# Performance work log

Hardware: AMD Instinct MI355X
Metric: run time of the kernel (lower is better)

Reference implementation:

```python
import jax, jax.numpy as jnp
import numpy as np

WIN = 7            # window side -> K2 = 49
DIM = 512          # channel dim C
HEADS = 16
E = DIM // HEADS   # embed_dim / head_dim = 32
SCALE = E ** -0.5


def _rel_pos_index(wh, ww):
    coords = np.stack(np.meshgrid(np.arange(wh), np.arange(ww), indexing='ij'))  # [2, wh, ww]
    cf = coords.reshape(2, -1)                      # [2, K2]
    rel = cf[:, :, None] - cf[:, None, :]           # [2, K2, K2]
    rel = rel.transpose(1, 2, 0).astype(np.int64)   # [K2, K2, 2]
    rel[..., 0] += wh - 1
    rel[..., 1] += ww - 1
    rel[..., 0] *= 2 * ww - 1
    return rel.sum(-1)                              # [K2, K2]

RPI = jnp.asarray(_rel_pos_index(WIN, WIN))         # constant int index map


def setup_inputs() -> dict:
    key = jax.random.key(0)
    ks = jax.random.split(key, 9)
    s = 0.02
    return {
        'x':         jax.random.normal(ks[0], (2048, WIN * WIN, DIM), jnp.float32),
        'qk_w':      jax.random.normal(ks[1], (2 * DIM, DIM), jnp.float32) * s,
        'qk_b':      jnp.zeros((2 * DIM,), jnp.float32),
        'rev_v_w':   jax.random.normal(ks[2], (DIM, DIM), jnp.float32) * s,
        'rev_v_b':   jnp.zeros((DIM,), jnp.float32),
        'wg_w':      jax.random.normal(ks[3], (E * E, DIM), jnp.float32) * s,
        'proj_w':    jax.random.normal(ks[4], (DIM, DIM), jnp.float32) * s,
        'proj_b':    jnp.zeros((DIM,), jnp.float32),
        'rpb_table': jax.random.normal(ks[5], ((2 * WIN - 1) ** 2, HEADS), jnp.float32) * s,
    }


def reference(x, qk_w, qk_b, rev_v_w, rev_v_b, wg_w, proj_w, proj_b, rpb_table):
    BW, K2, C = x.shape
    # joint q/k projection: [BW, K2, 2, H, E]
    qk = (x @ qk_w.T + qk_b).reshape(BW, K2, 2, HEADS, E)
    q = qk[:, :, 0].transpose(0, 2, 1, 3) * SCALE   # [BW, H, K2, E]
    k = qk[:, :, 1].transpose(0, 2, 1, 3)           # [BW, H, K2, E]
    attn = jnp.einsum('bhqe,bhke->bhqk', q, k)      # [BW, H, K2, K2]
    # relative position bias gather: [K2, K2, H] -> [H, K2, K2]
    bias = rpb_table[RPI].transpose(2, 0, 1)
    attn = jax.nn.softmax(attn + bias[None], axis=-1)
    # reverse attention: values projected, softmax transposed (transpose_softmax=True)
    v = (x @ rev_v_w.T + rev_v_b).reshape(BW, K2, HEADS, E).transpose(0, 2, 1, 3)  # [BW, H, K2, E]
    expert_mixture = jnp.einsum('bhkq,bhke->bhqe', attn, v)   # attn^T @ v, [BW, H, K2, E]
    # hypernetwork: per-token E x E mixing matrices from the raw input
    proj_weight = (x @ wg_w.T).reshape(BW, K2, E, E)          # [BW, K2, E, E]
    em_t = expert_mixture.transpose(0, 2, 1, 3)               # [BW, K2, H, E]
    out = jnp.einsum('bkhe,bkef->bkhf', em_t, proj_weight).reshape(BW, K2, C)
    # output projection (reverse_proj); dropouts are identity (p=0)
    return out @ proj_w.T + proj_b
```

## Files before the change

kernel.cpp:

```cpp
#include <hip/hip_runtime.h>
#include <hip/hip_bf16.h>
#include <stdint.h>

typedef __attribute__((ext_vector_type(8))) short short8;
typedef __attribute__((ext_vector_type(4))) float f32x4;
typedef unsigned short u16;

#define SCALE_F 0.17677669529663687f

__device__ __forceinline__ u16 f2bf(float f){
  union { float f; unsigned u; } x; x.f = f;
  unsigned r = x.u + 0x7fffu + ((x.u >> 16) & 1u);
  return (u16)(r >> 16);
}
__device__ __forceinline__ float bf2f(u16 u){
  union { float f; unsigned u; } x; x.u = ((unsigned)u) << 16; return x.f;
}
__device__ __forceinline__ unsigned swz(unsigned base, int row, unsigned rowb, unsigned colb){
  return base + (unsigned)row * rowb + (colb ^ (((unsigned)row & 7u) << 4));
}
__device__ __forceinline__ void gll16(const void* g, void* l){
  __builtin_amdgcn_global_load_lds(
    (const __attribute__((address_space(1))) unsigned int*)(unsigned long long)(size_t)g,
    (__attribute__((address_space(3))) unsigned int*)(unsigned int)(size_t)l,
    16, 0, 0);
}

__global__ void convk(const float* __restrict__ x,
                      const float* __restrict__ qk_w, const float* __restrict__ rev_v_w,
                      const float* __restrict__ wg_w, const float* __restrict__ proj_w,
                      u16* __restrict__ ws){
  long long i8 = ((long long)blockIdx.x * 256 + threadIdx.x) * 8;
  const float* s;
  if      (i8 <  524288) s = qk_w   + i8;
  else if (i8 <  786432) s = rev_v_w + (i8 - 524288);
  else if (i8 < 1310720) s = wg_w   + (i8 - 786432);
  else if (i8 < 1572864) s = proj_w + (i8 - 1310720);
  else                   s = x      + (i8 - 1572864);
  f32x4 lo = *(const f32x4*)s, hi = *(const f32x4*)(s + 4);
  short8 v;
  v[0]=f2bf(lo[0]); v[1]=f2bf(lo[1]); v[2]=f2bf(lo[2]); v[3]=f2bf(lo[3]);
  v[4]=f2bf(hi[0]); v[5]=f2bf(hi[1]); v[6]=f2bf(hi[2]); v[7]=f2bf(hi[3]);
  *(short8*)(ws + i8) = v;
}

template<int NT, int F32OUT>
__global__ __launch_bounds__(256, 2)
void gemm128(const u16* __restrict__ A, int lda,
             const u16* __restrict__ B,
             const float* __restrict__ b0, const float* __restrict__ b1,
             void* __restrict__ Cg, int ldc){
  __shared__ __align__(16) unsigned char sm[32768];
  const int tid = threadIdx.x, wave = tid >> 6, lane = tid & 63;
  const int l15 = lane & 15, lg = lane >> 4;
  const int nwg = gridDim.x, bidr = blockIdx.x;
  const int q8 = nwg >> 3, r8 = nwg & 7, xc = bidr & 7, oo = bidr >> 3;
  const int wg = (xc < r8 ? xc * (q8 + 1) : r8 * (q8 + 1) + (xc - r8) * q8) + oo;
  const int bm = wg / NT, bn = wg % NT;
  const int wm = wave >> 1, wn = wave & 1;
  const f32x4 zf = {0.f, 0.f, 0.f, 0.f};
  f32x4 acc[4][4];
#pragma unroll
  for (int mt=0; mt<4; mt++)
#pragma unroll
    for (int nt=0; nt<4; nt++) acc[mt][nt] = zf;

  const u16* Ab = A + (size_t)bm * 128 * lda;
  const u16* Bb = B + (size_t)bn * 128 * 512;

  for (int ks = 0; ks < 8; ks++){
#pragma unroll
    for (int it = 0; it < 4; it++){
      int c = (wave*4 + it)*64 + lane;
      int r = c >> 3, cc = c & 7;
      int sc = cc ^ (r & 7);
      gll16(Ab + (size_t)r*lda + ks*64 + sc*8, sm + (unsigned)(wave*4 + it)*1024u);
      gll16(Bb + (size_t)r*512 + ks*64 + sc*8, sm + 16384u + (unsigned)(wave*4 + it)*1024u);
    }
    __syncthreads();
#pragma unroll
    for (int kk = 0; kk < 2; kk++){
      short8 aq[4], bq[4];
#pragma unroll
      for (int mt=0; mt<4; mt++){
        int r = wm*64 + mt*16 + l15;
        aq[mt] = *(const short8*)(sm + (unsigned)r*128u + (((unsigned)(kk*64 + lg*16)) ^ (((unsigned)r & 7u) << 4)));
      }
#pragma unroll
      for (int nt=0; nt<4; nt++){
        int r = wn*64 + nt*16 + l15;
        bq[nt] = *(const short8*)(sm + 16384u + (unsigned)r*128u + (((unsigned)(kk*64 + lg*16)) ^ (((unsigned)r & 7u) << 4)));
      }
#pragma unroll
      for (int mt=0; mt<4; mt++)
#pragma unroll
        for (int nt=0; nt<4; nt++)
          acc[mt][nt] = __builtin_amdgcn_mfma_f32_16x16x32_bf16(aq[mt], bq[nt], acc[mt][nt], 0, 0, 0);
    }
    __syncthreads();
  }

  float bia[4];
#pragma unroll
  for (int nt=0; nt<4; nt++){
    int n = bn*128 + wn*64 + nt*16 + l15;
    if (F32OUT) bia[nt] = b0[n];
    else        bia[nt] = (n < 1024) ? b0[n] : (n < 1536 ? b1[n - 1024] : 0.f);
  }

  if (!F32OUT){
#pragma unroll
    for (int mt=0; mt<4; mt++)
#pragma unroll
      for (int nt=0; nt<4; nt++)
#pragma unroll
        for (int i=0; i<4; i++){
          int row = wm*64 + mt*16 + lg*4 + i;
          unsigned colb = (unsigned)((wn*64 + nt*16 + l15) * 2);
          *(u16*)(sm + (unsigned)row*256u + (colb ^ (((unsigned)row & 7u) << 4))) = f2bf(acc[mt][nt][i] + bia[nt]);
        }
    __syncthreads();
    u16* Co = (u16*)Cg;
#pragma unroll
    for (int it=0; it<8; it++){
      int c = it*256 + tid;
      int r = c >> 4, cc = c & 15;
      short8 v = *(const short8*)(sm + (unsigned)r*256u + (((unsigned)(cc*16)) ^ (((unsigned)r & 7u) << 4)));
      *(short8*)(Co + (size_t)(bm*128 + r)*ldc + bn*128 + cc*8) = v;
    }
  } else {
    float* Co = (float*)Cg;
#pragma unroll
    for (int half=0; half<2; half++){
      if (wm == half){
#pragma unroll
        for (int mt=0; mt<4; mt++)
#pragma unroll
          for (int nt=0; nt<4; nt++)
#pragma unroll
            for (int i=0; i<4; i++){
              int row = mt*16 + lg*4 + i;
              unsigned colb = (unsigned)((wn*64 + nt*16 + l15) * 4);
              *(float*)(sm + (unsigned)row*512u + (colb ^ (((unsigned)row & 7u) << 4))) = acc[mt][nt][i] + bia[nt];
            }
      }
      __syncthreads();
#pragma unroll
      for (int it=0; it<8; it++){
        int c = it*256 + tid;
        int r = c >> 5, cc = c & 31;
        f32x4 v = *(const f32x4*)(sm + (unsigned)r*512u + (((unsigned)(cc*16)) ^ (((unsigned)r & 7u) << 4)));
        *(f32x4*)(Co + (size_t)(bm*128 + half*64 + r)*ldc + bn*128 + cc*4) = v;
      }
      __syncthreads();
    }
  }
}

__global__ __launch_bounds__(512, 4)
void attn_half(const u16* __restrict__ qkv, const float* __restrict__ rpb,
               u16* __restrict__ em){
  __shared__ __align__(16) unsigned char lds[77968];
  const unsigned L_V = 0u, L_PT = 25088u, L_RPB = 75264u;
  const int tid = threadIdx.x, wave = tid >> 6, lane = tid & 63;
  const int l15 = lane & 15, lg = lane >> 4;
  const int bid = blockIdx.x, win = bid >> 1, hf = bid & 1;
  const u16* base = qkv + (size_t)win * 49 * 2560;
  u16* emb = em + (size_t)win * 49 * 512 + hf * 256;
  unsigned char* ptb = lds + L_PT + (unsigned)wave * 6272u;
  const int h = hf*8 + wave;
  const f32x4 zf = {0.f, 0.f, 0.f, 0.f};

  for (int i = tid; i < 169*8; i += 512){
    int idx = i >> 3, hh = i & 7;
    *(u16*)(lds + L_RPB + i*2) = f2bf(rpb[idx*16 + hf*8 + hh]);
  }
  for (int c = tid; c < 49*32; c += 512){
    int r = c >> 5, c8 = c & 31;
    short8 v = *(const short8*)(base + (size_t)r*2560 + 1024 + hf*256 + c8*8);
    *(short8*)(lds + swz(L_V, r, 512u, (unsigned)(c8*16))) = v;
  }
  __syncthreads();

  short8 aq[4], bq[4];
#pragma unroll
  for (int mt=0; mt<4; mt++){
    int r = mt*16 + l15; if (r > 48) r = 48;
    aq[mt] = *(const short8*)(base + (size_t)r*2560 + h*32 + lg*8);
  }
#pragma unroll
  for (int nt=0; nt<4; nt++){
    int kt = nt*16 + l15; if (kt > 48) kt = 48;
    bq[nt] = *(const short8*)(base + (size_t)kt*2560 + 512 + h*32 + lg*8);
  }
  f32x4 s[4][4];
#pragma unroll
  for (int mt=0; mt<4; mt++)
#pragma unroll
    for (int nt=0; nt<4; nt++) s[mt][nt] = zf;
#pragma unroll
  for (int mt=0; mt<4; mt++)
#pragma unroll
    for (int nt=0; nt<4; nt++)
      s[mt][nt] = __builtin_amdgcn_mfma_f32_16x16x32_bf16(aq[mt], bq[nt], s[mt][nt], 0, 0, 0);
#pragma unroll
  for (int mt=0; mt<4; mt++)
#pragma unroll
    for (int nt=0; nt<4; nt++)
#pragma unroll
      for (int i=0; i<4; i++){
        int q  = mt*16 + lg*4 + i;
        int kt = nt*16 + l15;
        float v = s[mt][nt][i] * SCALE_F;
        if (kt < 49){
          int qc = (q > 48) ? 48 : q;
          int qi = qc / 7, qj = qc - qi*7;
          int ki = kt / 7, kj = kt - ki*7;
          int idx = (qi - ki + 6)*13 + (qj - kj + 6);
          v += bf2f(*(const u16*)(lds + L_RPB + (idx*8 + wave)*2));
        } else v = -1e30f;
        s[mt][nt][i] = v;
      }
#pragma unroll
  for (int mt=0; mt<4; mt++)
#pragma unroll
    for (int i=0; i<4; i++){
      float m = fmaxf(fmaxf(s[mt][0][i], s[mt][1][i]), fmaxf(s[mt][2][i], s[mt][3][i]));
      m = fmaxf(m, __shfl_xor(m, 1)); m = fmaxf(m, __shfl_xor(m, 2));
      m = fmaxf(m, __shfl_xor(m, 4)); m = fmaxf(m, __shfl_xor(m, 8));
      float sum = 0.f;
#pragma unroll
      for (int nt=0; nt<4; nt++){ float e = __expf(s[mt][nt][i] - m); s[mt][nt][i] = e; sum += e; }
      sum += __shfl_xor(sum, 1); sum += __shfl_xor(sum, 2);
      sum += __shfl_xor(sum, 4); sum += __shfl_xor(sum, 8);
      float inv = 1.0f / sum;
#pragma unroll
      for (int nt=0; nt<4; nt++) s[mt][nt][i] *= inv;
    }
#pragma unroll
  for (int mt=0; mt<4; mt++)
#pragma unroll
    for (int nt=0; nt<4; nt++)
#pragma unroll
      for (int i=0; i<4; i++){
        int q  = mt*16 + lg*4 + i;
        int kt = nt*16 + l15;
        if (kt < 49){
          u16 val = (q < 49) ? f2bf(s[mt][nt][i]) : (u16)0;
          *(u16*)(ptb + (unsigned)kt*128u + (((unsigned)(q*2)) ^ (((unsigned)kt & 7u) << 4))) = val;
        }
      }
  f32x4 emv[4][2];
#pragma unroll
  for (int mt=0; mt<4; mt++)
#pragma unroll
    for (int nt=0; nt<2; nt++) emv[mt][nt] = zf;
#pragma unroll
  for (int kk=0; kk<2; kk++){
    short8 pa[4];
#pragma unroll
    for (int mt=0; mt<4; mt++){
      int r = mt*16 + l15; if (r > 48) r = 48;
      pa[mt] = *(const short8*)(ptb + (unsigned)r*128u + (((unsigned)(kk*64 + lg*16)) ^ (((unsigned)r & 7u) << 4)));
    }
    short8 vb[2];
#pragma unroll
    for (int nt=0; nt<2; nt++){
      int chl = wave*32 + nt*16 + l15;
#pragma unroll
      for (int j=0; j<8; j++){
        int kt = kk*32 + lg*8 + j; if (kt > 48) kt = 48;
        vb[nt][j] = *(const short*)(lds + swz(L_V, kt, 512u, (unsigned)(chl*2)));
      }
    }
#pragma unroll
    for (int mt=0; mt<4; mt++)
#pragma unroll
      for (int nt=0; nt<2; nt++)
        emv[mt][nt] = __builtin_amdgcn_mfma_f32_16x16x32_bf16(pa[mt], vb[nt], emv[mt][nt], 0, 0, 0);
  }
#pragma unroll
  for (int mt=0; mt<4; mt++)
#pragma unroll
    for (int nt=0; nt<2; nt++)
#pragma unroll
      for (int i=0; i<4; i++){
        int q = mt*16 + lg*4 + i;
        if (q < 49)
          emb[(size_t)q*512 + wave*32 + nt*16 + l15] = f2bf(emv[mt][nt][i]);
      }
}

__global__ __launch_bounds__(512, 4)
void hyper2(const u16* __restrict__ qkvpw, const u16* __restrict__ em,
            u16* __restrict__ o1){
  __shared__ __align__(16) unsigned char lds[16384];
  const int tid = threadIdx.x, wave = tid >> 6, lane = tid & 63;
  const int l15 = lane & 15, lg = lane >> 4;
  unsigned char* pwb = lds + (unsigned)wave * 2048u;
  const size_t t = (size_t)blockIdx.x * 8 + wave;
  const u16* pwt = qkvpw + t*2560 + 1536;
  const u16* emt = em + t*512;
  const f32x4 zf = {0.f, 0.f, 0.f, 0.f};

#pragma unroll
  for (int rd = 0; rd < 2; rd++){
    int i8 = (rd*64 + lane)*8;
    short8 v = *(const short8*)(pwt + i8);
    int e = i8 >> 5, f0 = i8 & 31;
#pragma unroll
    for (int jj = 0; jj < 8; jj++){
      int f = f0 + jj;
      *(u16*)(pwb + (unsigned)f*64u + (((unsigned)(e*2)) ^ (((unsigned)f & 3u) << 4))) = (u16)v[jj];
    }
  }
  short8 ea = *(const short8*)(emt + l15*32 + lg*8);
  __syncthreads();
  f32x4 o[2];
#pragma unroll
  for (int nt=0; nt<2; nt++){
    int f = nt*16 + l15;
    short8 pb = *(const short8*)(pwb + (unsigned)f*64u + (((unsigned)(lg*16)) ^ (((unsigned)f & 3u) << 4)));
    o[nt] = __builtin_amdgcn_mfma_f32_16x16x32_bf16(ea, pb, zf, 0, 0, 0);
  }
  __syncthreads();
#pragma unroll
  for (int nt=0; nt<2; nt++)
#pragma unroll
    for (int i=0; i<4; i++){
      int ch = (lg*4 + i)*32 + nt*16 + l15;
      *(u16*)(pwb + (unsigned)ch*2u) = f2bf(o[nt][i]);
    }
  __syncthreads();
  short8 v = *(const short8*)(pwb + (unsigned)lane*16u);
  *(short8*)(o1 + t*512 + lane*8) = v;
}

#define LDS_X   0u
#define LDS_V   50176u
#define LDS_QK  100352u
#define LDS_RPB 150528u
#define LDS_PW  50176u
#define LDS_EM  0u
#define LDS_TOTAL 155936

__device__ __forceinline__ void gemm_strip(const unsigned char* ldsp, unsigned abase,
    const u16* __restrict__ W, int wrow0, int l15, int lg, f32x4 acc[4][4]){
  for (int kk = 0; kk < 16; kk++){
    short8 bq[4];
#pragma unroll
    for (int nt = 0; nt < 4; nt++){
      const u16* p = W + (size_t)(wrow0 + nt*16 + l15) * 512 + kk*32 + lg*8;
      bq[nt] = *(const short8*)p;
    }
    short8 aq[4];
#pragma unroll
    for (int mt = 0; mt < 4; mt++){
      int r = mt*16 + l15; if (r > 48) r = 48;
      aq[mt] = *(const short8*)(ldsp + swz(abase, r, 1024u, (unsigned)(kk*64 + lg*16)));
    }
#pragma unroll
    for (int mt = 0; mt < 4; mt++)
#pragma unroll
      for (int nt = 0; nt < 4; nt++)
        acc[mt][nt] = __builtin_amdgcn_mfma_f32_16x16x32_bf16(aq[mt], bq[nt], acc[mt][nt], 0, 0, 0);
  }
}

__global__ void conv_w4(const float* __restrict__ a, const float* __restrict__ b,
                        const float* __restrict__ c, const float* __restrict__ d,
                        u16* __restrict__ o){
  int i = blockIdx.x * 256 + threadIdx.x;
  if (i < 524288)        o[i] = f2bf(a[i]);
  else if (i < 786432)   o[i] = f2bf(b[i - 524288]);
  else if (i < 1310720)  o[i] = f2bf(c[i - 786432]);
  else                   o[i] = f2bf(d[i - 1310720]);
}

__launch_bounds__(512, 2)
__global__ void wa_main(
    const float* __restrict__ x, const float* __restrict__ qk_b,
    const float* __restrict__ rev_v_b, const float* __restrict__ proj_b,
    const float* __restrict__ rpb,
    const u16* __restrict__ Wqk, const u16* __restrict__ Wv,
    const u16* __restrict__ Wwg, const u16* __restrict__ Wproj,
    float* __restrict__ out){
  __shared__ __align__(16) unsigned char ldsp[LDS_TOTAL];
  const int tid  = threadIdx.x;
  const int wave = tid >> 6, lane = tid & 63, l15 = lane & 15, lg = lane >> 4;
  const int b = blockIdx.x;
  const float* xb = x + (size_t)b * 49 * 512;
  const f32x4 zf = {0.f, 0.f, 0.f, 0.f};
  for (int i = tid; i < 169*16; i += 512)
    *(u16*)(ldsp + LDS_RPB + i*2) = f2bf(rpb[i]);
  for (int ch = tid; ch < 49*64; ch += 512){
    int r = ch >> 6, c8 = ch & 63;
    const f32x4* s = (const f32x4*)(xb + r*512 + c8*8);
    f32x4 lo = s[0], hi = s[1];
    short8 v;
    v[0]=f2bf(lo[0]); v[1]=f2bf(lo[1]); v[2]=f2bf(lo[2]); v[3]=f2bf(lo[3]);
    v[4]=f2bf(hi[0]); v[5]=f2bf(hi[1]); v[6]=f2bf(hi[2]); v[7]=f2bf(hi[3]);
    *(short8*)(ldsp + swz(LDS_X, r, 1024u, (unsigned)(c8*16))) = v;
  }
  __syncthreads();
  {
    f32x4 acc[4][4];
#pragma unroll
    for (int mt=0; mt<4; mt++)
#pragma unroll
      for (int nt=0; nt<4; nt++) acc[mt][nt] = zf;
    gemm_strip(ldsp, LDS_X, Wv, wave*64, l15, lg, acc);
#pragma unroll
    for (int nt=0; nt<4; nt++){
      int ch = wave*64 + nt*16 + l15;
      float bias = rev_v_b[ch];
#pragma unroll
      for (int mt=0; mt<4; mt++)
#pragma unroll
        for (int i=0; i<4; i++){
          int r = mt*16 + lg*4 + i;
          if (r < 49)
            *(u16*)(ldsp + swz(LDS_V, r, 1024u, (unsigned)(ch*2))) = f2bf(acc[mt][nt][i] + bias);
        }
    }
  }
  auto qk_pass = [&](int p){
    f32x4 acc[4][4];
#pragma unroll
    for (int mt=0; mt<4; mt++)
#pragma unroll
      for (int nt=0; nt<4; nt++) acc[mt][nt] = zf;
    int wrow0 = (wave < 4) ? (p*256 + wave*64) : (512 + p*256 + (wave-4)*64);
    gemm_strip(ldsp, LDS_X, Wqk, wrow0, l15, lg, acc);
#pragma unroll
    for (int nt=0; nt<4; nt++){
      int ch  = wrow0 + nt*16 + l15;
      int col = wave*64 + nt*16 + l15;
      float bias = qk_b[ch];
#pragma unroll
      for (int mt=0; mt<4; mt++)
#pragma unroll
        for (int i=0; i<4; i++){
          int r = mt*16 + lg*4 + i;
          if (r < 49)
            *(u16*)(ldsp + swz(LDS_QK, r, 1024u, (unsigned)(col*2))) = f2bf(acc[mt][nt][i] + bias);
        }
    }
  };
  auto attn_pass = [&](int p, f32x4 (&em)[4][2]){
    const int h = p*8 + wave;
    f32x4 s[4][4];
#pragma unroll
    for (int mt=0; mt<4; mt++)
#pragma unroll
      for (int nt=0; nt<4; nt++) s[mt][nt] = zf;
    short8 aq[4], bq[4];
#pragma unroll
    for (int mt=0; mt<4; mt++){
      int r = mt*16 + l15; if (r > 48) r = 48;
      aq[mt] = *(const short8*)(ldsp + swz(LDS_QK, r, 1024u, (unsigned)(wave*64 + lg*16)));
    }
#pragma unroll
    for (int nt=0; nt<4; nt++){
      int kt = nt*16 + l15; if (kt > 48) kt = 48;
      bq[nt] = *(const short8*)(ldsp + swz(LDS_QK, kt, 1024u, (unsigned)(512 + wave*64 + lg*16)));
    }
#pragma unroll
    for (int mt=0; mt<4; mt++)
#pragma unroll
      for (int nt=0; nt<4; nt++)
        s[mt][nt] = __builtin_amdgcn_mfma_f32_16x16x32_bf16(aq[mt], bq[nt], s[mt][nt], 0, 0, 0);
#pragma unroll
    for (int mt=0; mt<4; mt++)
#pragma unroll
      for (int nt=0; nt<4; nt++)
#pragma unroll
        for (int i=0; i<4; i++){
          int q  = mt*16 + lg*4 + i;
          int kt = nt*16 + l15;
          float v = s[mt][nt][i] * SCALE_F;
          if (kt < 49){
            int qc = (q > 48) ? 48 : q;
            int qi = qc / 7, qj = qc - qi*7;
            int ki = kt / 7, kj = kt - ki*7;
            int idx = (qi - ki + 6)*13 + (qj - kj + 6);
            v += bf2f(*(const u16*)(ldsp + LDS_RPB + (idx*16 + h)*2));
          } else v = -1e30f;
          s[mt][nt][i] = v;
        }
#pragma unroll
    for (int mt=0; mt<4; mt++)
#pragma unroll
      for (int i=0; i<4; i++){
        float m = fmaxf(fmaxf(s[mt][0][i], s[mt][1][i]), fmaxf(s[mt][2][i], s[mt][3][i]));
        m = fmaxf(m, __shfl_xor(m, 1)); m = fmaxf(m, __shfl_xor(m, 2));
        m = fmaxf(m, __shfl_xor(m, 4)); m = fmaxf(m, __shfl_xor(m, 8));
        float sum = 0.f;
#pragma unroll
        for (int nt=0; nt<4; nt++){ float e = __expf(s[mt][nt][i] - m); s[mt][nt][i] = e; sum += e; }
        sum += __shfl_xor(sum, 1); sum += __shfl_xor(sum, 2);
        sum += __shfl_xor(sum, 4); sum += __shfl_xor(sum, 8);
        float inv = 1.0f / sum;
#pragma unroll
        for (int nt=0; nt<4; nt++) s[mt][nt][i] *= inv;
      }
    __syncthreads();
    const unsigned ptb = LDS_QK + (unsigned)wave * 6272u;
#pragma unroll
    for (int mt=0; mt<4; mt++)
#pragma unroll
      for (int nt=0; nt<4; nt++)
#pragma unroll
        for (int i=0; i<4; i++){
          int q  = mt*16 + lg*4 + i;
          int kt = nt*16 + l15;
          if (kt < 49){
            u16 val = (q < 49) ? f2bf(s[mt][nt][i]) : (u16)0;
            *(u16*)(ldsp + ptb + (unsigned)kt*128u + (((unsigned)(q*2)) ^ (((unsigned)kt & 7u) << 4))) = val;
          }
        }
#pragma unroll
    for (int kk=0; kk<2; kk++){
      short8 pa[4];
#pragma unroll
      for (int mt=0; mt<4; mt++){
        int r = mt*16 + l15; if (r > 48) r = 48;
        pa[mt] = *(const short8*)(ldsp + ptb + (unsigned)r*128u + (((unsigned)(kk*64 + lg*16)) ^ (((unsigned)r & 7u) << 4)));
      }
      short8 vb[2];
#pragma unroll
      for (int nt=0; nt<2; nt++){
        int ch = h*32 + nt*16 + l15;
#pragma unroll
        for (int j=0; j<8; j++){
          int kt = kk*32 + lg*8 + j; if (kt > 48) kt = 48;
          vb[nt][j] = *(const short*)(ldsp + swz(LDS_V, kt, 1024u, (unsigned)(ch*2)));
        }
      }
#pragma unroll
      for (int mt=0; mt<4; mt++)
#pragma unroll
        for (int nt=0; nt<2; nt++)
          em[mt][nt] = __builtin_amdgcn_mfma_f32_16x16x32_bf16(pa[mt], vb[nt], em[mt][nt], 0, 0, 0);
    }
  };
  f32x4 em0[4][2], em1[4][2];
#pragma unroll
  for (int mt=0; mt<4; mt++)
#pragma unroll
    for (int nt=0; nt<2; nt++){ em0[mt][nt] = zf; em1[mt][nt] = zf; }
  qk_pass(0);
  __syncthreads();
  attn_pass(0, em0);
  __syncthreads();
  qk_pass(1);
  __syncthreads();
  attn_pass(1, em1);
  __syncthreads();
  for (int nh = 0; nh < 2; nh++){
    f32x4 acc[4][4];
#pragma unroll
    for (int mt=0; mt<4; mt++)
#pragma unroll
      for (int nt=0; nt<4; nt++) acc[mt][nt] = zf;
    int n0 = nh*512 + wave*64;
    gemm_strip(ldsp, LDS_X, Wwg, n0, l15, lg, acc);
#pragma unroll
    for (int nt=0; nt<4; nt++){
      int n  = n0 + nt*16 + l15;
      int pc = (n & 31)*32 + (n >> 5);
      unsigned cb = ((unsigned)(pc*2)) ^ (((unsigned)n & 7u) << 4);
#pragma unroll
      for (int mt=0; mt<4; mt++)
#pragma unroll
        for (int i=0; i<4; i++){
          int r = mt*16 + lg*4 + i;
          if (r < 49)
            *(u16*)(ldsp + LDS_PW + (unsigned)r*2048u + cb) = f2bf(acc[mt][nt][i]);
        }
    }
  }
  __syncthreads();
  auto em_store = [&](f32x4 (&em)[4][2], int h){
#pragma unroll
    for (int mt=0; mt<4; mt++)
#pragma unroll
      for (int nt=0; nt<2; nt++)
#pragma unroll
        for (int i=0; i<4; i++){
          int q = mt*16 + lg*4 + i;
          if (q < 49){
            int ch = h*32 + nt*16 + l15;
            *(u16*)(ldsp + swz(LDS_EM, q, 1024u, (unsigned)(ch*2))) = f2bf(em[mt][nt][i]);
          }
        }
  };
  em_store(em0, wave);
  em_store(em1, 8 + wave);
  __syncthreads();
  for (int t = wave; t < 49; t += 8){
    short8 ea = *(const short8*)(ldsp + swz(LDS_EM, t, 1024u, (unsigned)(l15*64 + lg*16)));
    f32x4 o[2];
#pragma unroll
    for (int nt=0; nt<2; nt++){
      int f = nt*16 + l15;
      short8 pb = *(const short8*)(ldsp + LDS_PW + (unsigned)t*2048u +
                    (((unsigned)((f*32 + lg*8)*2)) ^ (((unsigned)f & 7u) << 4)));
      o[nt] = __builtin_amdgcn_mfma_f32_16x16x32_bf16(ea, pb, zf, 0, 0, 0);
    }
#pragma unroll
    for (int nt=0; nt<2; nt++)
#pragma unroll
      for (int i=0; i<4; i++){
        int h2 = lg*4 + i;
        int ch = h2*32 + nt*16 + l15;
        *(u16*)(ldsp + swz(LDS_EM, t, 1024u, (unsigned)(ch*2))) = f2bf(o[nt][i]);
      }
  }
  __syncthreads();
  {
    f32x4 acc[4][4];
#pragma unroll
    for (int mt=0; mt<4; mt++)
#pragma unroll
      for (int nt=0; nt<4; nt++) acc[mt][nt] = zf;
    gemm_strip(ldsp, LDS_EM, Wproj, wave*64, l15, lg, acc);
    float* ob = out + (size_t)b * 49 * 512;
#pragma unroll
    for (int nt=0; nt<4; nt++){
      int n = wave*64 + nt*16 + l15;
      float bias = proj_b[n];
#pragma unroll
      for (int mt=0; mt<4; mt++)
#pragma unroll
        for (int i=0; i<4; i++){
          int r = mt*16 + lg*4 + i;
          if (r < 49) ob[r*512 + n] = acc[mt][nt][i] + bias;
        }
    }
  }
}

extern "C" void kernel_launch(void* const* d_in, const int* in_sizes, int n_in,
                              void* d_out, int out_size, void* d_ws, size_t ws_size,
                              hipStream_t stream){
  const float* x       = (const float*)d_in[0];
  const float* qk_w    = (const float*)d_in[1];
  const float* qk_b    = (const float*)d_in[2];
  const float* rev_v_w = (const float*)d_in[3];
  const float* rev_v_b = (const float*)d_in[4];
  const float* wg_w    = (const float*)d_in[5];
  const float* proj_w  = (const float*)d_in[6];
  const float* proj_b  = (const float*)d_in[7];
  const float* rpb     = (const float*)d_in[8];
  u16* ws = (u16*)d_ws;

  const unsigned long long BASE = 105906176ULL;
  int C = 0;
  for (int cand : {512, 1024, 2048, 256, 128}){
    if (BASE + (unsigned long long)cand * 351232ULL <= ws_size){ C = cand; break; }
  }
  if (C == 0){
    conv_w4<<<6144, 256, 0, stream>>>(qk_w, rev_v_w, wg_w, proj_w, ws);
    wa_main<<<2048, 512, 0, stream>>>(x, qk_b, rev_v_b, proj_b, rpb,
        ws, ws + 524288, ws + 786432, ws + 1310720, (float*)d_out);
    return;
  }

  u16* Wcat  = ws;
  u16* Wproj = ws + 1310720;
  u16* xb    = ws + 1572864;
  u16* qkvpw = ws + 52953088ULL;
  u16* o1    = qkvpw + (size_t)C * 49 * 2560;
  u16* em    = o1 + (size_t)C * 49 * 512;

  convk<<<25856, 256, 0, stream>>>(x, qk_w, rev_v_w, wg_w, proj_w, ws);

  const int nch = 2048 / C;
  const int mt128 = C * 49 / 128;
  for (int ch = 0; ch < nch; ch++){
    size_t t0 = (size_t)ch * C * 49;
    gemm128<20, 0><<<mt128 * 20, 256, 0, stream>>>(xb + t0*512, 512, Wcat,
        qk_b, rev_v_b, qkvpw, 2560);
    attn_half<<<2 * C, 512, 0, stream>>>(qkvpw, rpb, em);
    hyper2<<<C * 49 / 8, 512, 0, stream>>>(qkvpw, em, o1);
    gemm128<4, 1><<<mt128 * 4, 256, 0, stream>>>(o1, 512, Wproj,
        proj_b, (const float*)nullptr, (float*)d_out + t0*512, 512);
  }
  (void)Wcat; (void)Wproj;
}
```

Baseline: 666.2 us.

## Fuse hypernetwork mixing into attention kernel, keeping expert mixture in LDS

Removes the separate hyper2 kernel. Each attn_half2 block now writes its expert-mixture tile to shared memory, then loops over the window's 49 tokens. For each token it loads the per-token E×E mixing matrix, runs the small MFMA and writes o1 directly. This cuts the global round-trip of the em buffer and one kernel launch per chunk, and shrinks the workspace requirement. In exchange, both head-halves of a window reload the same per-token mixing matrix, and each wave processes tokens serially inside the block.

```diff
diff --git a/kernel.cpp b/kernel.cpp
--- a/kernel.cpp
+++ b/kernel.cpp
@@ -3,6 +3,7 @@
 #include <stdint.h>
 
 typedef __attribute__((ext_vector_type(8))) short short8;
+typedef __attribute__((ext_vector_type(4))) short s16x4;
 typedef __attribute__((ext_vector_type(4))) float f32x4;
 typedef unsigned short u16;
 
@@ -158,15 +159,14 @@
 }
 
 __global__ __launch_bounds__(512, 4)
-void attn_half(const u16* __restrict__ qkv, const float* __restrict__ rpb,
-               u16* __restrict__ em){
+void attn_half2(const u16* __restrict__ qkv, const float* __restrict__ rpb,
+                u16* __restrict__ o1){
   __shared__ __align__(16) unsigned char lds[77968];
   const unsigned L_V = 0u, L_PT = 25088u, L_RPB = 75264u;
   const int tid = threadIdx.x, wave = tid >> 6, lane = tid & 63;
   const int l15 = lane & 15, lg = lane >> 4;
   const int bid = blockIdx.x, win = bid >> 1, hf = bid & 1;
   const u16* base = qkv + (size_t)win * 49 * 2560;
-  u16* emb = em + (size_t)win * 49 * 512 + hf * 256;
   unsigned char* ptb = lds + L_PT + (unsigned)wave * 6272u;
   const int h = hf*8 + wave;
   const f32x4 zf = {0.f, 0.f, 0.f, 0.f};
@@ -279,6 +279,8 @@
       for (int nt=0; nt<2; nt++)
         emv[mt][nt] = __builtin_amdgcn_mfma_f32_16x16x32_bf16(pa[mt], vb[nt], emv[mt][nt], 0, 0, 0);
   }
+
+  __syncthreads();
 #pragma unroll
   for (int mt=0; mt<4; mt++)
 #pragma unroll
@@ -286,54 +288,46 @@
 #pragma unroll
       for (int i=0; i<4; i++){
         int q = mt*16 + lg*4 + i;
-        if (q < 49)
-          emb[(size_t)q*512 + wave*32 + nt*16 + l15] = f2bf(emv[mt][nt][i]);
-      }
-}
-
-__global__ __launch_bounds__(512, 4)
-void hyper2(const u16* __restrict__ qkvpw, const u16* __restrict__ em,
-            u16* __restrict__ o1){
-  __shared__ __align__(16) unsigned char lds[16384];
-  const int tid = threadIdx.x, wave = tid >> 6, lane = tid & 63;
-  const int l15 = lane & 15, lg = lane >> 4;
-  unsigned char* pwb = lds + (unsigned)wave * 2048u;
-  const size_t t = (size_t)blockIdx.x * 8 + wave;
-  const u16* pwt = qkvpw + t*2560 + 1536;
-  const u16* emt = em + t*512;
-  const f32x4 zf = {0.f, 0.f, 0.f, 0.f};
-
-#pragma unroll
-  for (int rd = 0; rd < 2; rd++){
-    int i8 = (rd*64 + lane)*8;
-    short8 v = *(const short8*)(pwt + i8);
-    int e = i8 >> 5, f0 = i8 & 31;
-#pragma unroll
-    for (int jj = 0; jj < 8; jj++){
-      int f = f0 + jj;
-      *(u16*)(pwb + (unsigned)f*64u + (((unsigned)(e*2)) ^ (((unsigned)f & 3u) << 4))) = (u16)v[jj];
-    }
-  }
-  short8 ea = *(const short8*)(emt + l15*32 + lg*8);
-  __syncthreads();
-  f32x4 o[2];
-#pragma unroll
-  for (int nt=0; nt<2; nt++){
-    int f = nt*16 + l15;
-    short8 pb = *(const short8*)(pwb + (unsigned)f*64u + (((unsigned)(lg*16)) ^ (((unsigned)f & 3u) << 4)));
-    o[nt] = __builtin_amdgcn_mfma_f32_16x16x32_bf16(ea, pb, zf, 0, 0, 0);
-  }
-  __syncthreads();
-#pragma unroll
-  for (int nt=0; nt<2; nt++)
-#pragma unroll
-    for (int i=0; i<4; i++){
-      int ch = (lg*4 + i)*32 + nt*16 + l15;
-      *(u16*)(pwb + (unsigned)ch*2u) = f2bf(o[nt][i]);
-    }
-  __syncthreads();
-  short8 v = *(const short8*)(pwb + (unsigned)lane*16u);
-  *(short8*)(o1 + t*512 + lane*8) = v;
+        if (q < 49){
+          int ch2 = wave*32 + nt*16 + l15;
+          *(u16*)(lds + swz(L_PT, q, 1024u, (unsigned)(ch2*2))) = f2bf(emv[mt][nt][i]);
+        }
+      }
+  __syncthreads();
+
+  unsigned char* pwb = lds + L_V + (unsigned)wave * 2048u;
+  u16* ob = o1 + (size_t)win * 49 * 512 + hf * 256;
+  for (int t = wave; t < 49; t += 8){
+    const u16* pwt = base + (size_t)t*2560 + 1536;
+#pragma unroll
+    for (int rd = 0; rd < 2; rd++){
+      int i8 = (rd*64 + lane)*8;
+      short8 v = *(const short8*)(pwt + i8);
+      int e = i8 >> 5, f0 = i8 & 31;
+#pragma unroll
+      for (int jj = 0; jj < 8; jj++){
+        int f = f0 + jj;
+        *(u16*)(pwb + (unsigned)f*64u + (((unsigned)(e*2)) ^ (((unsigned)f & 3u) << 4))) = (u16)v[jj];
+      }
+    }
+    short8 ea = *(const short8*)(lds + swz(L_PT, t, 1024u, (unsigned)(l15*64 + lg*16)));
+    f32x4 o[2];
+#pragma unroll
+    for (int nt2=0; nt2<2; nt2++){
+      int f = nt2*16 + l15;
+      short8 pb = *(const short8*)(pwb + (unsigned)f*64u + (((unsigned)(lg*16)) ^ (((unsigned)f & 3u) << 4)));
+      o[nt2] = __builtin_amdgcn_mfma_f32_16x16x32_bf16(ea, pb, zf, 0, 0, 0);
+    }
+#pragma unroll
+    for (int nt2=0; nt2<2; nt2++)
+#pragma unroll
+      for (int i=0; i<4; i++){
+        int ch2 = (lg*4 + i)*32 + nt2*16 + l15;
+        *(u16*)(pwb + (unsigned)ch2*2u) = f2bf(o[nt2][i]);
+      }
+    s16x4 ov = *(const s16x4*)(pwb + (unsigned)lane*8u);
+    *(s16x4*)(ob + (size_t)t*512 + lane*4) = ov;
+  }
 }
 
 #define LDS_X   0u
@@ -658,7 +652,7 @@
   const unsigned long long BASE = 105906176ULL;
   int C = 0;
   for (int cand : {512, 1024, 2048, 256, 128}){
-    if (BASE + (unsigned long long)cand * 351232ULL <= ws_size){ C = cand; break; }
+    if (BASE + (unsigned long long)cand * 301056ULL <= ws_size){ C = cand; break; }
   }
   if (C == 0){
     conv_w4<<<6144, 256, 0, stream>>>(qk_w, rev_v_w, wg_w, proj_w, ws);
@@ -672,7 +666,6 @@
   u16* xb    = ws + 1572864;
   u16* qkvpw = ws + 52953088ULL;
   u16* o1    = qkvpw + (size_t)C * 49 * 2560;
-  u16* em    = o1 + (size_t)C * 49 * 512;
 
   convk<<<25856, 256, 0, stream>>>(x, qk_w, rev_v_w, wg_w, proj_w, ws);
 
@@ -682,8 +675,7 @@
     size_t t0 = (size_t)ch * C * 49;
     gemm128<20, 0><<<mt128 * 20, 256, 0, stream>>>(xb + t0*512, 512, Wcat,
         qk_b, rev_v_b, qkvpw, 2560);
-    attn_half<<<2 * C, 512, 0, stream>>>(qkvpw, rpb, em);
-    hyper2<<<C * 49 / 8, 512, 0, stream>>>(qkvpw, em, o1);
+    attn_half2<<<2 * C, 512, 0, stream>>>(qkvpw, rpb, o1);
     gemm128<4, 1><<<mt128 * 4, 256, 0, stream>>>(o1, 512, Wproj,
         proj_b, (const float*)nullptr, (float*)d_out + t0*512, 512);
   }
```

New measurement: 678.5 us. About the same (+1.9%).

## Add 256x256 pipelined GEMM for fused QKV/hypernet projection, drop fallback path

Applied to the files above, without the earlier changes.

Adds a 512-thread GEMM kernel with 256x256 output tiles, double-buffered global-to-LDS direct loads, XOR-swizzled LDS, barrier-phased MFMA with priority bumps, and an LDS-staged coalesced epilogue. It replaces the 128x128 GEMM for the large projection when the row count divides by 256, aiming for more operand reuse and better load/compute overlap. It also removes the old fused single-kernel fallback and the C=2048 chunk option. The larger tile uses 128KB of dynamic LDS and allows one block per CU, which lowers occupancy.

```diff
diff --git a/kernel.cpp b/kernel.cpp
--- a/kernel.cpp
+++ b/kernel.cpp
@@ -44,6 +44,131 @@
   *(short8*)(ws + i8) = v;
 }
 
+template<int NT>
+__global__ __launch_bounds__(512, 1)
+void gemm256p(const u16* __restrict__ A,
+              const u16* __restrict__ B,
+              const float* __restrict__ b0, const float* __restrict__ b1,
+              u16* __restrict__ Cg, int ldc){
+  extern __shared__ __align__(16) unsigned char dyn[];
+  const int tid = threadIdx.x, wave = tid >> 6, lane = tid & 63;
+  const int l15 = lane & 15, lg = lane >> 4;
+  const int nwg = gridDim.x, bidr = blockIdx.x;
+  const int q8 = nwg >> 3, r8 = nwg & 7, xc = bidr & 7, oo = bidr >> 3;
+  const int wg = (xc < r8 ? xc*(q8+1) : r8*(q8+1) + (xc-r8)*q8) + oo;
+  const int bm = wg / NT, bn = wg % NT;
+  const int wm = wave >> 2, wn = wave & 3;
+  const f32x4 zf = {0.f, 0.f, 0.f, 0.f};
+
+  float bia[4];
+#pragma unroll
+  for (int nf=0; nf<4; nf++){
+    int n = bn*256 + wn*64 + nf*16 + l15;
+    bia[nf] = (n < 1024) ? b0[n] : (n < 1536 ? b1[n-1024] : 0.f);
+  }
+  asm volatile("s_waitcnt vmcnt(0)" ::: "memory");
+
+  const u16* Ab = A + (size_t)bm * 256 * 512;
+  const u16* Bb = B + (size_t)bn * 256 * 512;
+
+  const int c0 = tid, c1 = 512 + tid;
+  const int r0s = c0 >> 3, sc0 = (c0 & 7) ^ (r0s & 7);
+  const int r1s = c1 >> 3, sc1 = (c1 & 7) ^ (r1s & 7);
+
+  auto stageA = [&](int t, int h){
+    unsigned slot = ((unsigned)(t & 1)*2u + (unsigned)h) * 16384u;
+    const u16* src = Ab + (size_t)(h*128) * 512 + t*64;
+    gll16(src + (size_t)r0s*512 + sc0*8, dyn + slot + (unsigned)c0*16u);
+    gll16(src + (size_t)r1s*512 + sc1*8, dyn + slot + (unsigned)c1*16u);
+  };
+  auto stageB = [&](int t, int h){
+    unsigned slot = 65536u + ((unsigned)(t & 1)*2u + (unsigned)h) * 16384u;
+    const u16* src = Bb + (size_t)(h*128) * 512 + t*64;
+    gll16(src + (size_t)r0s*512 + sc0*8, dyn + slot + (unsigned)c0*16u);
+    gll16(src + (size_t)r1s*512 + sc1*8, dyn + slot + (unsigned)c1*16u);
+  };
+
+  f32x4 acc[8][4];
+#pragma unroll
+  for (int mf=0; mf<8; mf++)
+#pragma unroll
+    for (int nf=0; nf<4; nf++) acc[mf][nf] = zf;
+
+  stageA(0,0); stageA(0,1); stageB(0,0); stageB(0,1); stageB(1,0); stageB(1,1);
+  asm volatile("s_waitcnt vmcnt(4)" ::: "memory");
+  __builtin_amdgcn_s_barrier();
+  __builtin_amdgcn_sched_barrier(0);
+
+  short8 bq[4][2];
+  for (int t = 0; t < 8; t++){
+    const unsigned aslot = ((unsigned)(t&1)*2u + (unsigned)wm) * 16384u;
+    const unsigned bslot = 65536u + ((unsigned)(t&1)*2u + (unsigned)(wn>>1)) * 16384u;
+    const int brow = (wn & 1)*64;
+#pragma unroll
+    for (int p = 0; p < 4; p++){
+      short8 aq[2][2];
+#pragma unroll
+      for (int j=0; j<2; j++)
+#pragma unroll
+        for (int kk=0; kk<2; kk++){
+          int rl = p*32 + j*16 + l15;
+          aq[j][kk] = *(const short8*)(dyn + aslot + (unsigned)rl*128u +
+                        (((unsigned)(kk*64 + lg*16)) ^ (((unsigned)rl & 7u) << 4)));
+        }
+      if (p == 0){
+#pragma unroll
+        for (int nf=0; nf<4; nf++)
+#pragma unroll
+          for (int kk=0; kk<2; kk++){
+            int rl = brow + nf*16 + l15;
+            bq[nf][kk] = *(const short8*)(dyn + bslot + (unsigned)rl*128u +
+                          (((unsigned)(kk*64 + lg*16)) ^ (((unsigned)rl & 7u) << 4)));
+          }
+      }
+      if (p < 2){ if (t+1 < 8) stageA(t+1, p); }
+      else      { if (t+2 < 8) stageB(t+2, p-2); }
+      if (p == 3){
+        if (t <= 5)      asm volatile("s_waitcnt vmcnt(4)" ::: "memory");
+        else if (t == 6) asm volatile("s_waitcnt vmcnt(0)" ::: "memory");
+      }
+      __builtin_amdgcn_s_barrier();
+      __builtin_amdgcn_sched_barrier(0);
+      __builtin_amdgcn_s_setprio(1);
+#pragma unroll
+      for (int j=0; j<2; j++)
+#pragma unroll
+        for (int nf=0; nf<4; nf++)
+#pragma unroll
+          for (int kk=0; kk<2; kk++)
+            acc[p*2+j][nf] = __builtin_amdgcn_mfma_f32_16x16x32_bf16(
+                                aq[j][kk], bq[nf][kk], acc[p*2+j][nf], 0, 0, 0);
+      __builtin_amdgcn_s_setprio(0);
+      __builtin_amdgcn_s_barrier();
+      __builtin_amdgcn_sched_barrier(0);
+    }
+  }
+
+  __syncthreads();
+#pragma unroll
+  for (int mf=0; mf<8; mf++)
+#pragma unroll
+    for (int nf=0; nf<4; nf++)
+#pragma unroll
+      for (int i=0; i<4; i++){
+        int row = wm*128 + mf*16 + lg*4 + i;
+        unsigned colb = (unsigned)((wn*64 + nf*16 + l15) * 2);
+        *(u16*)(dyn + (unsigned)row*512u + (colb ^ (((unsigned)row & 7u) << 4))) = f2bf(acc[mf][nf][i] + bia[nf]);
+      }
+  __syncthreads();
+#pragma unroll
+  for (int it=0; it<16; it++){
+    int c = it*512 + tid;
+    int r = c >> 5, cc = c & 31;
+    short8 v = *(const short8*)(dyn + (unsigned)r*512u + (((unsigned)(cc*16)) ^ (((unsigned)r & 7u) << 4)));
+    *(short8*)(Cg + (size_t)(bm*256 + r)*ldc + bn*256 + cc*8) = v;
+  }
+}
+
 template<int NT, int F32OUT>
 __global__ __launch_bounds__(256, 2)
 void gemm128(const u16* __restrict__ A, int lda,
@@ -336,311 +461,6 @@
   *(short8*)(o1 + t*512 + lane*8) = v;
 }
 
-#define LDS_X   0u
-#define LDS_V   50176u
-#define LDS_QK  100352u
-#define LDS_RPB 150528u
-#define LDS_PW  50176u
-#define LDS_EM  0u
-#define LDS_TOTAL 155936
-
-__device__ __forceinline__ void gemm_strip(const unsigned char* ldsp, unsigned abase,
-    const u16* __restrict__ W, int wrow0, int l15, int lg, f32x4 acc[4][4]){
-  for (int kk = 0; kk < 16; kk++){
-    short8 bq[4];
-#pragma unroll
-    for (int nt = 0; nt < 4; nt++){
-      const u16* p = W + (size_t)(wrow0 + nt*16 + l15) * 512 + kk*32 + lg*8;
-      bq[nt] = *(const short8*)p;
-    }
-    short8 aq[4];
-#pragma unroll
-    for (int mt = 0; mt < 4; mt++){
-      int r = mt*16 + l15; if (r > 48) r = 48;
-      aq[mt] = *(const short8*)(ldsp + swz(abase, r, 1024u, (unsigned)(kk*64 + lg*16)));
-    }
-#pragma unroll
-    for (int mt = 0; mt < 4; mt++)
-#pragma unroll
-      for (int nt = 0; nt < 4; nt++)
-        acc[mt][nt] = __builtin_amdgcn_mfma_f32_16x16x32_bf16(aq[mt], bq[nt], acc[mt][nt], 0, 0, 0);
-  }
-}
-
-__global__ void conv_w4(const float* __restrict__ a, const float* __restrict__ b,
-                        const float* __restrict__ c, const float* __restrict__ d,
-                        u16* __restrict__ o){
-  int i = blockIdx.x * 256 + threadIdx.x;
-  if (i < 524288)        o[i] = f2bf(a[i]);
-  else if (i < 786432)   o[i] = f2bf(b[i - 524288]);
-  else if (i < 1310720)  o[i] = f2bf(c[i - 786432]);
-  else                   o[i] = f2bf(d[i - 1310720]);
-}
-
-__launch_bounds__(512, 2)
-__global__ void wa_main(
-    const float* __restrict__ x, const float* __restrict__ qk_b,
-    const float* __restrict__ rev_v_b, const float* __restrict__ proj_b,
-    const float* __restrict__ rpb,
-    const u16* __restrict__ Wqk, const u16* __restrict__ Wv,
-    const u16* __restrict__ Wwg, const u16* __restrict__ Wproj,
-    float* __restrict__ out){
-  __shared__ __align__(16) unsigned char ldsp[LDS_TOTAL];
-  const int tid  = threadIdx.x;
-  const int wave = tid >> 6, lane = tid & 63, l15 = lane & 15, lg = lane >> 4;
-  const int b = blockIdx.x;
-  const float* xb = x + (size_t)b * 49 * 512;
-  const f32x4 zf = {0.f, 0.f, 0.f, 0.f};
-  for (int i = tid; i < 169*16; i += 512)
-    *(u16*)(ldsp + LDS_RPB + i*2) = f2bf(rpb[i]);
-  for (int ch = tid; ch < 49*64; ch += 512){
-    int r = ch >> 6, c8 = ch & 63;
-    const f32x4* s = (const f32x4*)(xb + r*512 + c8*8);
-    f32x4 lo = s[0], hi = s[1];
-    short8 v;
-    v[0]=f2bf(lo[0]); v[1]=f2bf(lo[1]); v[2]=f2bf(lo[2]); v[3]=f2bf(lo[3]);
-    v[4]=f2bf(hi[0]); v[5]=f2bf(hi[1]); v[6]=f2bf(hi[2]); v[7]=f2bf(hi[3]);
-    *(short8*)(ldsp + swz(LDS_X, r, 1024u, (unsigned)(c8*16))) = v;
-  }
-  __syncthreads();
-  {
-    f32x4 acc[4][4];
-#pragma unroll
-    for (int mt=0; mt<4; mt++)
-#pragma unroll
-      for (int nt=0; nt<4; nt++) acc[mt][nt] = zf;
-    gemm_strip(ldsp, LDS_X, Wv, wave*64, l15, lg, acc);
-#pragma unroll
-    for (int nt=0; nt<4; nt++){
-      int ch = wave*64 + nt*16 + l15;
-      float bias = rev_v_b[ch];
-#pragma unroll
-      for (int mt=0; mt<4; mt++)
-#pragma unroll
-        for (int i=0; i<4; i++){
-          int r = mt*16 + lg*4 + i;
-          if (r < 49)
-            *(u16*)(ldsp + swz(LDS_V, r, 1024u, (unsigned)(ch*2))) = f2bf(acc[mt][nt][i] + bias);
-        }
-    }
-  }
-  auto qk_pass = [&](int p){
-    f32x4 acc[4][4];
-#pragma unroll
-    for (int mt=0; mt<4; mt++)
-#pragma unroll
-      for (int nt=0; nt<4; nt++) acc[mt][nt] = zf;
-    int wrow0 = (wave < 4) ? (p*256 + wave*64) : (512 + p*256 + (wave-4)*64);
-    gemm_strip(ldsp, LDS_X, Wqk, wrow0, l15, lg, acc);
-#pragma unroll
-    for (int nt=0; nt<4; nt++){
-      int ch  = wrow0 + nt*16 + l15;
-      int col = wave*64 + nt*16 + l15;
-      float bias = qk_b[ch];
-#pragma unroll
-      for (int mt=0; mt<4; mt++)
-#pragma unroll
-        for (int i=0; i<4; i++){
-          int r = mt*16 + lg*4 + i;
-          if (r < 49)
-            *(u16*)(ldsp + swz(LDS_QK, r, 1024u, (unsigned)(col*2))) = f2bf(acc[mt][nt][i] + bias);
-        }
-    }
-  };
-  auto attn_pass = [&](int p, f32x4 (&em)[4][2]){
-    const int h = p*8 + wave;
-    f32x4 s[4][4];
-#pragma unroll
-    for (int mt=0; mt<4; mt++)
-#pragma unroll
-      for (int nt=0; nt<4; nt++) s[mt][nt] = zf;
-    short8 aq[4], bq[4];
-#pragma unroll
-    for (int mt=0; mt<4; mt++){
-      int r = mt*16 + l15; if (r > 48) r = 48;
-      aq[mt] = *(const short8*)(ldsp + swz(LDS_QK, r, 1024u, (unsigned)(wave*64 + lg*16)));
-    }
-#pragma unroll
-    for (int nt=0; nt<4; nt++){
-      int kt = nt*16 + l15; if (kt > 48) kt = 48;
-      bq[nt] = *(const short8*)(ldsp + swz(LDS_QK, kt, 1024u, (unsigned)(512 + wave*64 + lg*16)));
-    }
-#pragma unroll
-    for (int mt=0; mt<4; mt++)
-#pragma unroll
-      for (int nt=0; nt<4; nt++)
-        s[mt][nt] = __builtin_amdgcn_mfma_f32_16x16x32_bf16(aq[mt], bq[nt], s[mt][nt], 0, 0, 0);
-#pragma unroll
-    for (int mt=0; mt<4; mt++)
-#pragma unroll
-      for (int nt=0; nt<4; nt++)
-#pragma unroll
-        for (int i=0; i<4; i++){
-          int q  = mt*16 + lg*4 + i;
-          int kt = nt*16 + l15;
-          float v = s[mt][nt][i] * SCALE_F;
-          if (kt < 49){
-            int qc = (q > 48) ? 48 : q;
-            int qi = qc / 7, qj = qc - qi*7;
-            int ki = kt / 7, kj = kt - ki*7;
-            int idx = (qi - ki + 6)*13 + (qj - kj + 6);
-            v += bf2f(*(const u16*)(ldsp + LDS_RPB + (idx*16 + h)*2));
-          } else v = -1e30f;
-          s[mt][nt][i] = v;
-        }
-#pragma unroll
-    for (int mt=0; mt<4; mt++)
-#pragma unroll
-      for (int i=0; i<4; i++){
-        float m = fmaxf(fmaxf(s[mt][0][i], s[mt][1][i]), fmaxf(s[mt][2][i], s[mt][3][i]));
-        m = fmaxf(m, __shfl_xor(m, 1)); m = fmaxf(m, __shfl_xor(m, 2));
-        m = fmaxf(m, __shfl_xor(m, 4)); m = fmaxf(m, __shfl_xor(m, 8));
-        float sum = 0.f;
-#pragma unroll
-        for (int nt=0; nt<4; nt++){ float e = __expf(s[mt][nt][i] - m); s[mt][nt][i] = e; sum += e; }
-        sum += __shfl_xor(sum, 1); sum += __shfl_xor(sum, 2);
-        sum += __shfl_xor(sum, 4); sum += __shfl_xor(sum, 8);
-        float inv = 1.0f / sum;
-#pragma unroll
-        for (int nt=0; nt<4; nt++) s[mt][nt][i] *= inv;
-      }
-    __syncthreads();
-    const unsigned ptb = LDS_QK + (unsigned)wave * 6272u;
-#pragma unroll
-    for (int mt=0; mt<4; mt++)
-#pragma unroll
-      for (int nt=0; nt<4; nt++)
-#pragma unroll
-        for (int i=0; i<4; i++){
-          int q  = mt*16 + lg*4 + i;
-          int kt = nt*16 + l15;
-          if (kt < 49){
-            u16 val = (q < 49) ? f2bf(s[mt][nt][i]) : (u16)0;
-            *(u16*)(ldsp + ptb + (unsigned)kt*128u + (((unsigned)(q*2)) ^ (((unsigned)kt & 7u) << 4))) = val;
-          }
-        }
-#pragma unroll
-    for (int kk=0; kk<2; kk++){
-      short8 pa[4];
-#pragma unroll
-      for (int mt=0; mt<4; mt++){
-        int r = mt*16 + l15; if (r > 48) r = 48;
-        pa[mt] = *(const short8*)(ldsp + ptb + (unsigned)r*128u + (((unsigned)(kk*64 + lg*16)) ^ (((unsigned)r & 7u) << 4)));
-      }
-      short8 vb[2];
-#pragma unroll
-      for (int nt=0; nt<2; nt++){
-        int ch = h*32 + nt*16 + l15;
-#pragma unroll
-        for (int j=0; j<8; j++){
-          int kt = kk*32 + lg*8 + j; if (kt > 48) kt = 48;
-          vb[nt][j] = *(const short*)(ldsp + swz(LDS_V, kt, 1024u, (unsigned)(ch*2)));
-        }
-      }
-#pragma unroll
-      for (int mt=0; mt<4; mt++)
-#pragma unroll
-        for (int nt=0; nt<2; nt++)
-          em[mt][nt] = __builtin_amdgcn_mfma_f32_16x16x32_bf16(pa[mt], vb[nt], em[mt][nt], 0, 0, 0);
-    }
-  };
-  f32x4 em0[4][2], em1[4][2];
-#pragma unroll
-  for (int mt=0; mt<4; mt++)
-#pragma unroll
-    for (int nt=0; nt<2; nt++){ em0[mt][nt] = zf; em1[mt][nt] = zf; }
-  qk_pass(0);
-  __syncthreads();
-  attn_pass(0, em0);
-  __syncthreads();
-  qk_pass(1);
-  __syncthreads();
-  attn_pass(1, em1);
-  __syncthreads();
-  for (int nh = 0; nh < 2; nh++){
-    f32x4 acc[4][4];
-#pragma unroll
-    for (int mt=0; mt<4; mt++)
-#pragma unroll
-      for (int nt=0; nt<4; nt++) acc[mt][nt] = zf;
-    int n0 = nh*512 + wave*64;
-    gemm_strip(ldsp, LDS_X, Wwg, n0, l15, lg, acc);
-#pragma unroll
-    for (int nt=0; nt<4; nt++){
-      int n  = n0 + nt*16 + l15;
-      int pc = (n & 31)*32 + (n >> 5);
-      unsigned cb = ((unsigned)(pc*2)) ^ (((unsigned)n & 7u) << 4);
-#pragma unroll
-      for (int mt=0; mt<4; mt++)
-#pragma unroll
-        for (int i=0; i<4; i++){
-          int r = mt*16 + lg*4 + i;
-          if (r < 49)
-            *(u16*)(ldsp + LDS_PW + (unsigned)r*2048u + cb) = f2bf(acc[mt][nt][i]);
-        }
-    }
-  }
-  __syncthreads();
-  auto em_store = [&](f32x4 (&em)[4][2], int h){
-#pragma unroll
-    for (int mt=0; mt<4; mt++)
-#pragma unroll
-      for (int nt=0; nt<2; nt++)
-#pragma unroll
-        for (int i=0; i<4; i++){
-          int q = mt*16 + lg*4 + i;
-          if (q < 49){
-            int ch = h*32 + nt*16 + l15;
-            *(u16*)(ldsp + swz(LDS_EM, q, 1024u, (unsigned)(ch*2))) = f2bf(em[mt][nt][i]);
-          }
-        }
-  };
-  em_store(em0, wave);
-  em_store(em1, 8 + wave);
-  __syncthreads();
-  for (int t = wave; t < 49; t += 8){
-    short8 ea = *(const short8*)(ldsp + swz(LDS_EM, t, 1024u, (unsigned)(l15*64 + lg*16)));
-    f32x4 o[2];
-#pragma unroll
-    for (int nt=0; nt<2; nt++){
-      int f = nt*16 + l15;
-      short8 pb = *(const short8*)(ldsp + LDS_PW + (unsigned)t*2048u +
-                    (((unsigned)((f*32 + lg*8)*2)) ^ (((unsigned)f & 7u) << 4)));
-      o[nt] = __builtin_amdgcn_mfma_f32_16x16x32_bf16(ea, pb, zf, 0, 0, 0);
-    }
-#pragma unroll
-    for (int nt=0; nt<2; nt++)
-#pragma unroll
-      for (int i=0; i<4; i++){
-        int h2 = lg*4 + i;
-        int ch = h2*32 + nt*16 + l15;
-        *(u16*)(ldsp + swz(LDS_EM, t, 1024u, (unsigned)(ch*2))) = f2bf(o[nt][i]);
-      }
-  }
-  __syncthreads();
-  {
-    f32x4 acc[4][4];
-#pragma unroll
-    for (int mt=0; mt<4; mt++)
-#pragma unroll
-      for (int nt=0; nt<4; nt++) acc[mt][nt] = zf;
-    gemm_strip(ldsp, LDS_EM, Wproj, wave*64, l15, lg, acc);
-    float* ob = out + (size_t)b * 49 * 512;
-#pragma unroll
-    for (int nt=0; nt<4; nt++){
-      int n = wave*64 + nt*16 + l15;
-      float bias = proj_b[n];
-#pragma unroll
-      for (int mt=0; mt<4; mt++)
-#pragma unroll
-        for (int i=0; i<4; i++){
-          int r = mt*16 + lg*4 + i;
-          if (r < 49) ob[r*512 + n] = acc[mt][nt][i] + bias;
-        }
-    }
-  }
-}
-
 extern "C" void kernel_launch(void* const* d_in, const int* in_sizes, int n_in,
                               void* d_out, int out_size, void* d_ws, size_t ws_size,
                               hipStream_t stream){
@@ -657,15 +477,10 @@
 
   const unsigned long long BASE = 105906176ULL;
   int C = 0;
-  for (int cand : {512, 1024, 2048, 256, 128}){
+  for (int cand : {512, 1024, 256, 128}){
     if (BASE + (unsigned long long)cand * 351232ULL <= ws_size){ C = cand; break; }
   }
-  if (C == 0){
-    conv_w4<<<6144, 256, 0, stream>>>(qk_w, rev_v_w, wg_w, proj_w, ws);
-    wa_main<<<2048, 512, 0, stream>>>(x, qk_b, rev_v_b, proj_b, rpb,
-        ws, ws + 524288, ws + 786432, ws + 1310720, (float*)d_out);
-    return;
-  }
+  if (C == 0) return;
 
   u16* Wcat  = ws;
   u16* Wproj = ws + 1310720;
@@ -676,12 +491,24 @@
 
   convk<<<25856, 256, 0, stream>>>(x, qk_w, rev_v_w, wg_w, proj_w, ws);
 
+  bool use256 = ((C * 49) % 256 == 0);
+  if (use256){
+    hipError_t e = hipFuncSetAttribute((const void*)gemm256p<10>,
+        hipFuncAttributeMaxDynamicSharedMemorySize, 131072);
+    if (e != hipSuccess) use256 = false;
+  }
+
   const int nch = 2048 / C;
   const int mt128 = C * 49 / 128;
+  const int mt256 = C * 49 / 256;
   for (int ch = 0; ch < nch; ch++){
     size_t t0 = (size_t)ch * C * 49;
-    gemm128<20, 0><<<mt128 * 20, 256, 0, stream>>>(xb + t0*512, 512, Wcat,
-        qk_b, rev_v_b, qkvpw, 2560);
+    if (use256)
+      gemm256p<10><<<mt256 * 10, 512, 131072, stream>>>(xb + t0*512, Wcat,
+          qk_b, rev_v_b, qkvpw, 2560);
+    else
+      gemm128<20, 0><<<mt128 * 20, 256, 0, stream>>>(xb + t0*512, 512, Wcat,
+          qk_b, rev_v_b, qkvpw, 2560);
     attn_half<<<2 * C, 512, 0, stream>>>(qkvpw, rpb, em);
     hyper2<<<C * 49 / 8, 512, 0, stream>>>(qkvpw, em, o1);
     gemm128<4, 1><<<mt128 * 4, 256, 0, stream>>>(o1, 512, Wproj,
```

New measurement: 667.3 us. No clear change (+0.2%).
